# Kernel tuning notes

Measured on AMD Instinct MI355X. Metric: run time of the kernel, lower is better.

The kernel has to match this reference:

```python
import jax, jax.numpy as jnp
import numpy as np
from jax import lax

B, N, T_IN, F_IN = 64, 800, 15, 8
T_OUT = 12
H = 64
NC = 9
KS = [2, 2, 2, 3, 3, 3, 4, 4, 4]
DS = [1, 2, 4, 1, 2, 4, 1, 2, 4]


def setup_inputs() -> dict:
    key = jax.random.key(0)
    ks = jax.random.split(key, 16)
    s = 0.1
    f32 = jnp.float32
    inp = {}
    inp['A'] = jnp.zeros((1,), f32)  # deprecated graph arg, unused
    inp['X'] = jax.random.normal(ks[0], (B, N, T_IN, F_IN), f32)
    # dilated conv weights grouped by kernel size (comps 0-2 k=2, 3-5 k=3, 6-8 k=4)
    inp['convw2'] = jax.random.normal(ks[1], (3, F_IN, F_IN, 2), f32) * s
    inp['convw3'] = jax.random.normal(ks[2], (3, F_IN, F_IN, 3), f32) * s
    inp['convw4'] = jax.random.normal(ks[3], (3, F_IN, F_IN, 4), f32) * s
    inp['convb'] = jax.random.normal(ks[4], (NC, F_IN), f32) * s
    # encoder GRU params (PyTorch layout: W_ih (3H,F), W_hh (3H,H))
    inp['enc_wih'] = jax.random.normal(ks[5], (NC, 3 * H, F_IN), f32) * s
    inp['enc_whh'] = jax.random.normal(ks[6], (NC, 3 * H, H), f32) * s
    inp['enc_bih'] = jax.random.normal(ks[7], (NC, 3 * H), f32) * s
    inp['enc_bhh'] = jax.random.normal(ks[8], (NC, 3 * H), f32) * s
    # decoder GRUCell params (input size 1)
    inp['dec_wih'] = jax.random.normal(ks[9], (NC, 3 * H, 1), f32) * s
    inp['dec_whh'] = jax.random.normal(ks[10], (NC, 3 * H, H), f32) * s
    inp['dec_bih'] = jax.random.normal(ks[11], (NC, 3 * H), f32) * s
    inp['dec_bhh'] = jax.random.normal(ks[12], (NC, 3 * H), f32) * s
    # per-comp readout Linear(H, 1)
    inp['lin_w'] = jax.random.normal(ks[13], (NC, 1, H), f32) * s
    inp['lin_b'] = jax.random.normal(ks[14], (NC, 1), f32) * s
    # node-wise component mixing embedding
    inp['embed'] = jax.random.normal(ks[15], (N, NC), f32)
    return inp


def gru_cell(x, h, wih, whh, bih, bhh):
    # PyTorch GRU semantics
    gi = x @ wih.T + bih  # (B, 3H)
    gh = h @ whh.T + bhh  # (B, 3H)
    ir, iz, in_ = jnp.split(gi, 3, axis=-1)
    hr, hz, hn = jnp.split(gh, 3, axis=-1)
    r = jax.nn.sigmoid(ir + hr)
    z = jax.nn.sigmoid(iz + hz)
    n = jnp.tanh(in_ + r * hn)
    return (1.0 - z) * n + z * h


def reference(A, X, convw2, convw3, convw4, convb, enc_wih, enc_whh, enc_bih,
              enc_bhh, dec_wih, dec_whh, dec_bih, dec_bhh, lin_w, lin_b, embed):
    del A  # deprecated in pure TS model
    Xf = X.reshape(-1, T_IN, F_IN)            # (B*N, T, F)
    xt = jnp.transpose(Xf, (0, 2, 1))         # (B*N, F, T) for conv NCH
    last0 = Xf[:, -1, 0:1]                    # X1[-1, :, 0] -> (B*N, 1)
    BN = Xf.shape[0]
    conv_ws = [convw2[0], convw2[1], convw2[2], convw3[0], convw3[1],
               convw3[2], convw4[0], convw4[1], convw4[2]]
    outs = []
    for r in range(NC):
        # dilated conv over time, VALID padding (length shrinks by d*(k-1))
        h = lax.conv_general_dilated(xt, conv_ws[r], (1,), 'VALID',
                                     rhs_dilation=(DS[r],),
                                     dimension_numbers=('NCH', 'OIH', 'NCH'))
        h = h + convb[r][None, :, None]
        seq = jnp.transpose(h, (2, 0, 1))     # time-major (L, B*N, F)

        ewih, ewhh, ebih, ebhh = enc_wih[r], enc_whh[r], enc_bih[r], enc_bhh[r]

        def enc_step(hc, x_t):
            return gru_cell(x_t, hc, ewih, ewhh, ebih, ebhh), None

        h_enc, _ = lax.scan(enc_step, jnp.zeros((BN, H), X.dtype), seq)

        dwih, dwhh, dbih, dbhh = dec_wih[r], dec_whh[r], dec_bih[r], dec_bhh[r]
        lw, lb = lin_w[r], lin_b[r]

        def dec_step(carry, _):
            hd, lv = carry
            hd = gru_cell(lv, hd, dwih, dwhh, dbih, dbhh)
            v = hd @ lw.T + lb                # (B*N, 1)
            # torch code feeds value.detach() back in
            return (hd, lax.stop_gradient(v)), v[:, 0]

        _, vals = lax.scan(dec_step, (h_enc, last0), None, length=T_OUT)
        outs.append(jnp.transpose(vals).reshape(B, N, T_OUT))  # (B, N, T_out)
    out = jnp.stack(outs, axis=-1)            # (B, N, T_out, NC)
    w = jax.nn.softmax(embed, axis=-1)        # (N, NC)
    return jnp.einsum('bntc,nc->bnt', out, w)
```

## Files before the change

kernel.cpp:

```cpp
#include <hip/hip_runtime.h>
#include <hip/hip_bf16.h>
#include <stdint.h>

typedef unsigned short u16;
typedef unsigned int   u32;
typedef float f32x4  __attribute__((ext_vector_type(4)));
typedef short bf16x8 __attribute__((ext_vector_type(8)));

#define NSEQ 800
#define TOUT 12
#define NC   9
#define LOG2E  1.44269504088896340736f
#define LOG2E2 2.88539008177792681472f

#define WIMG_STRIDE 73728
#define LDS_BHE 0
#define LDS_BXE 24576
#define LDS_BHD 36864
#define LDS_H   61440
#define LDS_TOTAL 77824
#define BIASE_OFF 663552
#define BIASD_OFF 672768
#define WGT_OFF   681984

__device__ __forceinline__ u16 f2bf(float f){ union{float f;u32 i;}v; v.f=f; u32 x=v.i; return (u16)((x + 0x7fffu + ((x>>16)&1u))>>16); }
__device__ __forceinline__ u32 pkbf(float a, float b){
  union{ __hip_bfloat162 h2; u32 u; } v;
  v.h2 = __float22bfloat162_rn(float2{a,b});
  return v.u;
}

union BXU { uint4 u; bf16x8 v; };

__global__ void prep_kernel(
  const float* __restrict__ cw2, const float* __restrict__ cw3, const float* __restrict__ cw4,
  const float* __restrict__ cbv,
  const float* __restrict__ Ewih, const float* __restrict__ Ewhh,
  const float* __restrict__ Ebih, const float* __restrict__ Ebhh,
  const float* __restrict__ Dwih, const float* __restrict__ Dwhh,
  const float* __restrict__ Dbih, const float* __restrict__ Dbhh,
  const float* __restrict__ emb,
  char* __restrict__ ws)
{
  const int r = blockIdx.x;
  const int tid = threadIdx.x;
  const int K = (r<3) ? 2 : ((r<6) ? 3 : 4);
  char* wimg = ws + (size_t)r*WIMG_STRIDE;

  const float* ewhh = Ewhh + (size_t)r*192*64;
  const float* dwhh = Dwhh + (size_t)r*192*64;
  #pragma unroll 1
  for (int s = tid; s < 1536; s += 512){
    int g = s >> 6, fl = s & 63;
    int ks = g/12, nt = g%12;
    int col = nt*16 + (fl&15);
    float sc = (nt<8) ? LOG2E : LOG2E2;
    u32 we[4] = {0,0,0,0}, wd[4] = {0,0,0,0};
    #pragma unroll
    for (int j=0;j<8;j++){
      int hid = ((j&3)<<4) | (ks*8 + (fl>>4)*2 + (j>>2));
      we[j>>1] |= (u32)f2bf(sc * ewhh[col*64 + hid]) << ((j&1)*16);
      wd[j>>1] |= (u32)f2bf(sc * dwhh[col*64 + hid]) << ((j&1)*16);
    }
    *(uint4*)(wimg + LDS_BHE + s*16) = uint4{we[0],we[1],we[2],we[3]};
    *(uint4*)(wimg + LDS_BHD + s*16) = uint4{wd[0],wd[1],wd[2],wd[3]};
  }
  const float* wih = Ewih + r*192*8;
  const float* cw  = (r<3) ? (cw2 + r*128) : (r<6) ? (cw3 + (r-3)*192) : (cw4 + (r-6)*256);
  #pragma unroll 1
  for (int s = tid; s < 768; s += 512){
    int g = s >> 6, fl = s & 63;
    int col = g*16 + (fl&15);
    int tap = fl>>4;
    float sc = (g<8) ? LOG2E : LOG2E2;
    u32 w[4] = {0,0,0,0};
    if (tap < K){
      #pragma unroll
      for (int j=0;j<8;j++){
        float a = 0.f;
        #pragma unroll
        for (int o=0;o<8;o++) a += wih[col*8+o]*cw[(o*8+j)*K + tap];
        w[j>>1] |= (u32)f2bf(sc*a) << ((j&1)*16);
      }
    }
    *(uint4*)(wimg + LDS_BXE + s*16) = uint4{w[0],w[1],w[2],w[3]};
  }
  if (tid < 16){
    int n = tid;
    const float* bi = Ebih + r*192; const float* bh2 = Ebhh + r*192;
    const float* cb = cbv + r*8;
    float* be = (float*)(ws + BIASE_OFF) + ((size_t)r*16 + n)*16;
    #pragma unroll
    for (int ht=0; ht<4; ht++){
      int hid = ht*16 + n;
      float cR=0.f,cZ=0.f,cN=0.f;
      #pragma unroll
      for (int o=0;o<8;o++){
        cR += wih[hid*8+o]*cb[o];
        cZ += wih[(64+hid)*8+o]*cb[o];
        cN += wih[(128+hid)*8+o]*cb[o];
      }
      be[ht]    = LOG2E  * (bi[hid]     + bh2[hid]     + cR);
      be[4+ht]  = LOG2E  * (bi[64+hid]  + bh2[64+hid]  + cZ);
      be[8+ht]  = LOG2E2 * (bi[128+hid]                + cN);
      be[12+ht] = LOG2E2 *                bh2[128+hid];
    }
  } else if (tid < 32){
    int n = tid - 16;
    const float* bi = Dbih + r*192; const float* bh2 = Dbhh + r*192;
    float* bd = (float*)(ws + BIASD_OFF) + ((size_t)r*16 + n)*16;
    #pragma unroll
    for (int ht=0; ht<4; ht++){
      int hid = ht*16 + n;
      bd[ht]    = LOG2E  * (bi[hid]     + bh2[hid]);
      bd[4+ht]  = LOG2E  * (bi[64+hid]  + bh2[64+hid]);
      bd[8+ht]  = LOG2E2 *  bi[128+hid];
      bd[12+ht] = LOG2E2 *  bh2[128+hid];
    }
  }
  if (r == 0){
    float* wg = (float*)(ws + WGT_OFF);
    #pragma unroll 1
    for (int nb = tid; nb < NSEQ; nb += 512){
      float e[NC], mx = -1e30f;
      #pragma unroll
      for (int c=0;c<NC;c++){ e[c] = emb[nb*NC+c]; mx = fmaxf(mx, e[c]); }
      float sm = 0.f;
      #pragma unroll
      for (int c=0;c<NC;c++){ e[c] = __expf(e[c]-mx); sm += e[c]; }
      float inv = 1.f/sm;
      #pragma unroll
      for (int c=0;c<NC;c++) wg[nb*NC+c] = e[c]*inv;
    }
  }
}

__global__ __launch_bounds__(512, 2) void rnn_kernel(
  const float* __restrict__ X,
  const float* __restrict__ Dwih,
  const float* __restrict__ Lw, const float* __restrict__ Lb,
  const char* __restrict__ ws,
  float* __restrict__ out)
{
  __shared__ char LDSC[LDS_TOTAL];
  const int tid = threadIdx.x;
  const int wv  = tid >> 6;
  const int l   = tid & 63;
  const int q   = l >> 4;
  const int n   = l & 15;
  const int r   = blockIdx.y;
  const int seqb = blockIdx.x*128 + wv*16;

  const int Kc[NC]={2,2,2,3,3,3,4,4,4};
  const int Dc[NC]={1,2,4,1,2,4,1,2,4};
  const int K = Kc[r], D = Dc[r];
  const int L = 15 - (K-1)*D;

  const int HB = LDS_H + wv*2048;
  *(uint4*)(LDSC + HB + l*32)      = uint4{0,0,0,0};
  *(uint4*)(LDSC + HB + l*32 + 16) = uint4{0,0,0,0};

  {
    const uint4* src = (const uint4*)(ws + (size_t)r*WIMG_STRIDE);
    #pragma unroll 1
    for (int it=0; it<8; it++){
      int idx = it*512 + tid;
      if (idx < 3840) *(uint4*)(LDSC + idx*16) = src[idx];
    }
  }

  float bR4[4], bZ4[4], bNi4[4], bNh4[4];
  {
    const float* be = (const float*)(ws + BIASE_OFF) + ((size_t)r*16 + n)*16;
    float4 v0 = *(const float4*)(be);
    float4 v1 = *(const float4*)(be+4);
    float4 v2 = *(const float4*)(be+8);
    float4 v3 = *(const float4*)(be+12);
    bR4[0]=v0.x; bR4[1]=v0.y; bR4[2]=v0.z; bR4[3]=v0.w;
    bZ4[0]=v1.x; bZ4[1]=v1.y; bZ4[2]=v1.z; bZ4[3]=v1.w;
    bNi4[0]=v2.x; bNi4[1]=v2.y; bNi4[2]=v2.z; bNi4[3]=v2.w;
    bNh4[0]=v3.x; bNh4[1]=v3.y; bNh4[2]=v3.z; bNh4[3]=v3.w;
  }

  float hO[4][4];
  #pragma unroll
  for (int ht=0;ht<4;ht++) for (int i=0;i<4;i++) hO[ht][i]=0.f;

  const int ra0 = HB + n*128 + (((  q + n)&7)<<4);
  const int ra1 = HB + n*128 + (((4+q + n)&7)<<4);
  int wa[4];
  #pragma unroll
  for (int i=0;i<4;i++){
    int seq = q*4+i;
    wa[i] = HB + seq*128 + ((((n>>1) + seq)&7)<<4) + ((n&1)<<3);
  }

#define POINTWISE(aR_,aZ_,aNi_,aNh_,HT) \
    _Pragma("unroll") \
    for (int i=0;i<4;i++){ \
      float Er = __builtin_amdgcn_exp2f(-aR_[i]); \
      float rr = __builtin_amdgcn_rcpf(1.f + Er); \
      float y  = aNi_[i] + rr*aNh_[i]; \
      float En = __builtin_amdgcn_exp2f(y); \
      float Ez = __builtin_amdgcn_exp2f(-aZ_[i]); \
      float h  = hO[HT][i]; \
      float e1 = En + 1.f; \
      float den = e1 + e1*Ez; \
      float num = En*(Ez+h) + (h-Ez); \
      float hn = num * __builtin_amdgcn_rcpf(den); \
      hO[HT][i] = hn; \
      if (HT==0)      hsv[i] = hn; \
      else if (HT==1) pk01[i] = pkbf(hsv[i], hn); \
      else if (HT==2) hsv[i] = hn; \
      else            pk23[i] = pkbf(hsv[i], hn); \
    }

  auto step_core = [&](bf16x8 ax){
    bf16x8 a0 = *(const bf16x8*)(LDSC + ra0);
    bf16x8 a1 = *(const bf16x8*)(LDSC + ra1);
    float hsv[4]; u32 pk01[4], pk23[4];
    #pragma unroll
    for (int ht=0; ht<4; ht++){
      bf16x8 bR0 = *(const bf16x8*)(LDSC + LDS_BHE + ((      ht)*64 + l)*16);
      bf16x8 bR1 = *(const bf16x8*)(LDSC + LDS_BHE + ((12  + ht)*64 + l)*16);
      bf16x8 bZ0 = *(const bf16x8*)(LDSC + LDS_BHE + (( 4 + ht)*64 + l)*16);
      bf16x8 bZ1 = *(const bf16x8*)(LDSC + LDS_BHE + ((16  + ht)*64 + l)*16);
      bf16x8 bN0 = *(const bf16x8*)(LDSC + LDS_BHE + (( 8 + ht)*64 + l)*16);
      bf16x8 bN1 = *(const bf16x8*)(LDSC + LDS_BHE + ((20  + ht)*64 + l)*16);
      bf16x8 xR  = *(const bf16x8*)(LDSC + LDS_BXE + ((      ht)*64 + l)*16);
      bf16x8 xZ  = *(const bf16x8*)(LDSC + LDS_BXE + (( 4 + ht)*64 + l)*16);
      bf16x8 xN  = *(const bf16x8*)(LDSC + LDS_BXE + (( 8 + ht)*64 + l)*16);
      f32x4 aR  = f32x4{bR4[ht],bR4[ht],bR4[ht],bR4[ht]};
      f32x4 aZ  = f32x4{bZ4[ht],bZ4[ht],bZ4[ht],bZ4[ht]};
      f32x4 aNi = f32x4{bNi4[ht],bNi4[ht],bNi4[ht],bNi4[ht]};
      f32x4 aNh = f32x4{bNh4[ht],bNh4[ht],bNh4[ht],bNh4[ht]};
      aR = __builtin_amdgcn_mfma_f32_16x16x32_bf16(a0, bR0, aR,0,0,0);
      aR = __builtin_amdgcn_mfma_f32_16x16x32_bf16(a1, bR1, aR,0,0,0);
      aR = __builtin_amdgcn_mfma_f32_16x16x32_bf16(ax, xR,  aR,0,0,0);
      aZ = __builtin_amdgcn_mfma_f32_16x16x32_bf16(a0, bZ0, aZ,0,0,0);
      aZ = __builtin_amdgcn_mfma_f32_16x16x32_bf16(a1, bZ1, aZ,0,0,0);
      aZ = __builtin_amdgcn_mfma_f32_16x16x32_bf16(ax, xZ,  aZ,0,0,0);
      aNh= __builtin_amdgcn_mfma_f32_16x16x32_bf16(a0, bN0, aNh,0,0,0);
      aNh= __builtin_amdgcn_mfma_f32_16x16x32_bf16(a1, bN1, aNh,0,0,0);
      aNi= __builtin_amdgcn_mfma_f32_16x16x32_bf16(ax, xN,  aNi,0,0,0);
      POINTWISE(aR,aZ,aNi,aNh,ht)
    }
    #pragma unroll
    for (int i=0;i<4;i++){
      uint2 wv2; wv2.x = pk01[i]; wv2.y = pk23[i];
      *(uint2*)(LDSC + wa[i]) = wv2;
    }
  };

  const float* xb = X + (size_t)(seqb + n)*120 + ((q<K)? q:0)*D*8;
  __syncthreads();
  #pragma unroll 1
  for (int t=0; t<L; t++){
    float4 v0 = *(const float4*)(xb + t*8);
    float4 v1 = *(const float4*)(xb + t*8 + 4);
    BXU a;
    a.u.x = __builtin_amdgcn_perm(__float_as_uint(v0.y), __float_as_uint(v0.x), 0x07060302u);
    a.u.y = __builtin_amdgcn_perm(__float_as_uint(v0.w), __float_as_uint(v0.z), 0x07060302u);
    a.u.z = __builtin_amdgcn_perm(__float_as_uint(v1.y), __float_as_uint(v1.x), 0x07060302u);
    a.u.w = __builtin_amdgcn_perm(__float_as_uint(v1.w), __float_as_uint(v1.z), 0x07060302u);
    step_core(a.v);
  }

  {
    const float* bd = (const float*)(ws + BIASD_OFF) + ((size_t)r*16 + n)*16;
    float4 v0 = *(const float4*)(bd);
    float4 v1 = *(const float4*)(bd+4);
    float4 v2 = *(const float4*)(bd+8);
    float4 v3 = *(const float4*)(bd+12);
    bR4[0]=v0.x; bR4[1]=v0.y; bR4[2]=v0.z; bR4[3]=v0.w;
    bZ4[0]=v1.x; bZ4[1]=v1.y; bZ4[2]=v1.z; bZ4[3]=v1.w;
    bNi4[0]=v2.x; bNi4[1]=v2.y; bNi4[2]=v2.z; bNi4[3]=v2.w;
    bNh4[0]=v3.x; bNh4[1]=v3.y; bNh4[2]=v3.z; bNh4[3]=v3.w;
  }
  float dwR[4], dwZ[4], dwN[4];
  {
    const float* dwih = Dwih + r*192;
    #pragma unroll
    for (int ht=0; ht<4; ht++){
      int hid = ht*16 + n;
      dwR[ht] = LOG2E  * dwih[hid];
      dwZ[ht] = LOG2E  * dwih[64+hid];
      dwN[ht] = LOG2E2 * dwih[128+hid];
    }
  }
  float lwr[4];
  #pragma unroll
  for (int ht=0; ht<4; ht++) lwr[ht] = Lw[r*64 + ht*16 + n];
  const float lb_ = Lb[r];
  const float wgt = ((const float*)(ws + WGT_OFF))[((seqb + q*4 + (n&3)) % NSEQ)*NC + r];
  f32x4 lvv;
  #pragma unroll
  for (int i=0;i<4;i++) lvv[i] = X[(size_t)(seqb + q*4 + i)*120 + 112];

  #pragma unroll 1
  for (int t=0; t<TOUT; t++){
    {
      bf16x8 a0 = *(const bf16x8*)(LDSC + ra0);
      bf16x8 a1 = *(const bf16x8*)(LDSC + ra1);
      float hsv[4]; u32 pk01[4], pk23[4];
      #pragma unroll
      for (int ht=0; ht<4; ht++){
        bf16x8 bR0 = *(const bf16x8*)(LDSC + LDS_BHD + ((      ht)*64 + l)*16);
        bf16x8 bR1 = *(const bf16x8*)(LDSC + LDS_BHD + ((12  + ht)*64 + l)*16);
        bf16x8 bZ0 = *(const bf16x8*)(LDSC + LDS_BHD + (( 4 + ht)*64 + l)*16);
        bf16x8 bZ1 = *(const bf16x8*)(LDSC + LDS_BHD + ((16  + ht)*64 + l)*16);
        bf16x8 bN0 = *(const bf16x8*)(LDSC + LDS_BHD + (( 8 + ht)*64 + l)*16);
        bf16x8 bN1 = *(const bf16x8*)(LDSC + LDS_BHD + ((20  + ht)*64 + l)*16);
        f32x4 aR, aZ, aNi, aNh;
        #pragma unroll
        for (int i=0;i<4;i++){
          aR[i]  = bR4[ht]  + lvv[i]*dwR[ht];
          aZ[i]  = bZ4[ht]  + lvv[i]*dwZ[ht];
          aNi[i] = bNi4[ht] + lvv[i]*dwN[ht];
          aNh[i] = bNh4[ht];
        }
        aR = __builtin_amdgcn_mfma_f32_16x16x32_bf16(a0, bR0, aR,0,0,0);
        aR = __builtin_amdgcn_mfma_f32_16x16x32_bf16(a1, bR1, aR,0,0,0);
        aZ = __builtin_amdgcn_mfma_f32_16x16x32_bf16(a0, bZ0, aZ,0,0,0);
        aZ = __builtin_amdgcn_mfma_f32_16x16x32_bf16(a1, bZ1, aZ,0,0,0);
        aNh= __builtin_amdgcn_mfma_f32_16x16x32_bf16(a0, bN0, aNh,0,0,0);
        aNh= __builtin_amdgcn_mfma_f32_16x16x32_bf16(a1, bN1, aNh,0,0,0);
        POINTWISE(aR,aZ,aNi,aNh,ht)
      }
      #pragma unroll
      for (int i=0;i<4;i++){
        uint2 wv2; wv2.x = pk01[i]; wv2.y = pk23[i];
        *(uint2*)(LDSC + wa[i]) = wv2;
      }
    }
    float p[4];
    #pragma unroll
    for (int i=0;i<4;i++)
      p[i] = hO[0][i]*lwr[0] + hO[1][i]*lwr[1] + hO[2][i]*lwr[2] + hO[3][i]*lwr[3];
    #pragma unroll
    for (int m=1; m<16; m<<=1){
      #pragma unroll
      for (int i=0;i<4;i++) p[i] += __shfl_xor(p[i], m, 64);
    }
    #pragma unroll
    for (int i=0;i<4;i++) lvv[i] = p[i] + lb_;
    if (n < 4){
      float vout = (n&2) ? ((n&1)? lvv[3] : lvv[2]) : ((n&1)? lvv[1] : lvv[0]);
      atomicAdd(out + (size_t)(seqb + q*4 + n)*TOUT + t, wgt*vout);
    }
  }
}

extern "C" void kernel_launch(void* const* d_in, const int* in_sizes, int n_in,
                              void* d_out, int out_size, void* d_ws, size_t ws_size,
                              hipStream_t stream)
{
  float* out = (float*)d_out;
  hipMemsetAsync(out, 0, (size_t)out_size*sizeof(float), stream);

  prep_kernel<<<dim3(NC), 512, 0, stream>>>(
    (const float*)d_in[2], (const float*)d_in[3], (const float*)d_in[4],
    (const float*)d_in[5],
    (const float*)d_in[6], (const float*)d_in[7], (const float*)d_in[8], (const float*)d_in[9],
    (const float*)d_in[10],(const float*)d_in[11],(const float*)d_in[12],(const float*)d_in[13],
    (const float*)d_in[16],
    (char*)d_ws);

  dim3 g(NSEQ*64/128, NC);
  rnn_kernel<<<g, 512, 0, stream>>>(
    (const float*)d_in[1],
    (const float*)d_in[10],
    (const float*)d_in[14], (const float*)d_in[15],
    (const char*)d_ws,
    out);
}
```

Baseline: 755.7 us.

## Halve block size and reuse one LDS region for encoder and decoder weights

The encoder and decoder recurrent weight images now share one LDS region. The decoder weights are reloaded from workspace after the encoder loop, with barriers around the reload. This cuts LDS per block from about 76KB to 44KB. Blocks shrink from 512 to 256 threads with launch bounds of 4 blocks per CU, doubling the grid, to raise occupancy and latency hiding. The costs are an extra global-to-LDS copy and two block barriers per block, plus twice as many encoder-weight loads overall.

```diff
diff --git a/kernel.cpp b/kernel.cpp
--- a/kernel.cpp
+++ b/kernel.cpp
@@ -14,11 +14,11 @@
 #define LOG2E2 2.88539008177792681472f
 
 #define WIMG_STRIDE 73728
-#define LDS_BHE 0
+#define WIMG_BHD 36864
+#define LDS_BH  0
 #define LDS_BXE 24576
-#define LDS_BHD 36864
-#define LDS_H   61440
-#define LDS_TOTAL 77824
+#define LDS_H   36864
+#define LDS_TOTAL 45056
 #define BIASE_OFF 663552
 #define BIASD_OFF 672768
 #define WGT_OFF   681984
@@ -62,8 +62,8 @@
       we[j>>1] |= (u32)f2bf(sc * ewhh[col*64 + hid]) << ((j&1)*16);
       wd[j>>1] |= (u32)f2bf(sc * dwhh[col*64 + hid]) << ((j&1)*16);
     }
-    *(uint4*)(wimg + LDS_BHE + s*16) = uint4{we[0],we[1],we[2],we[3]};
-    *(uint4*)(wimg + LDS_BHD + s*16) = uint4{wd[0],wd[1],wd[2],wd[3]};
+    *(uint4*)(wimg + LDS_BH + s*16)   = uint4{we[0],we[1],we[2],we[3]};
+    *(uint4*)(wimg + WIMG_BHD + s*16) = uint4{wd[0],wd[1],wd[2],wd[3]};
   }
   const float* wih = Ewih + r*192*8;
   const float* cw  = (r<3) ? (cw2 + r*128) : (r<6) ? (cw3 + (r-3)*192) : (cw4 + (r-6)*256);
@@ -135,7 +135,7 @@
   }
 }
 
-__global__ __launch_bounds__(512, 2) void rnn_kernel(
+__global__ __launch_bounds__(256, 4) void rnn_kernel(
   const float* __restrict__ X,
   const float* __restrict__ Dwih,
   const float* __restrict__ Lw, const float* __restrict__ Lb,
@@ -149,7 +149,7 @@
   const int q   = l >> 4;
   const int n   = l & 15;
   const int r   = blockIdx.y;
-  const int seqb = blockIdx.x*128 + wv*16;
+  const int seqb = blockIdx.x*64 + wv*16;
 
   const int Kc[NC]={2,2,2,3,3,3,4,4,4};
   const int Dc[NC]={1,2,4,1,2,4,1,2,4};
@@ -163,9 +163,9 @@
   {
     const uint4* src = (const uint4*)(ws + (size_t)r*WIMG_STRIDE);
     #pragma unroll 1
-    for (int it=0; it<8; it++){
-      int idx = it*512 + tid;
-      if (idx < 3840) *(uint4*)(LDSC + idx*16) = src[idx];
+    for (int it=0; it<9; it++){
+      int idx = it*256 + tid;
+      *(uint4*)(LDSC + idx*16) = src[idx];
     }
   }
 
@@ -221,12 +221,12 @@
     float hsv[4]; u32 pk01[4], pk23[4];
     #pragma unroll
     for (int ht=0; ht<4; ht++){
-      bf16x8 bR0 = *(const bf16x8*)(LDSC + LDS_BHE + ((      ht)*64 + l)*16);
-      bf16x8 bR1 = *(const bf16x8*)(LDSC + LDS_BHE + ((12  + ht)*64 + l)*16);
-      bf16x8 bZ0 = *(const bf16x8*)(LDSC + LDS_BHE + (( 4 + ht)*64 + l)*16);
-      bf16x8 bZ1 = *(const bf16x8*)(LDSC + LDS_BHE + ((16  + ht)*64 + l)*16);
-      bf16x8 bN0 = *(const bf16x8*)(LDSC + LDS_BHE + (( 8 + ht)*64 + l)*16);
-      bf16x8 bN1 = *(const bf16x8*)(LDSC + LDS_BHE + ((20  + ht)*64 + l)*16);
+      bf16x8 bR0 = *(const bf16x8*)(LDSC + LDS_BH + ((      ht)*64 + l)*16);
+      bf16x8 bR1 = *(const bf16x8*)(LDSC + LDS_BH + ((12  + ht)*64 + l)*16);
+      bf16x8 bZ0 = *(const bf16x8*)(LDSC + LDS_BH + (( 4 + ht)*64 + l)*16);
+      bf16x8 bZ1 = *(const bf16x8*)(LDSC + LDS_BH + ((16  + ht)*64 + l)*16);
+      bf16x8 bN0 = *(const bf16x8*)(LDSC + LDS_BH + (( 8 + ht)*64 + l)*16);
+      bf16x8 bN1 = *(const bf16x8*)(LDSC + LDS_BH + ((20  + ht)*64 + l)*16);
       bf16x8 xR  = *(const bf16x8*)(LDSC + LDS_BXE + ((      ht)*64 + l)*16);
       bf16x8 xZ  = *(const bf16x8*)(LDSC + LDS_BXE + (( 4 + ht)*64 + l)*16);
       bf16x8 xN  = *(const bf16x8*)(LDSC + LDS_BXE + (( 8 + ht)*64 + l)*16);
@@ -266,6 +266,15 @@
     step_core(a.v);
   }
 
+  __syncthreads();
+  {
+    const uint4* src = (const uint4*)(ws + (size_t)r*WIMG_STRIDE + WIMG_BHD);
+    #pragma unroll 1
+    for (int it=0; it<6; it++){
+      int idx = it*256 + tid;
+      *(uint4*)(LDSC + LDS_BH + idx*16) = src[idx];
+    }
+  }
   {
     const float* bd = (const float*)(ws + BIASD_OFF) + ((size_t)r*16 + n)*16;
     float4 v0 = *(const float4*)(bd);
@@ -296,6 +305,7 @@
   f32x4 lvv;
   #pragma unroll
   for (int i=0;i<4;i++) lvv[i] = X[(size_t)(seqb + q*4 + i)*120 + 112];
+  __syncthreads();
 
   #pragma unroll 1
   for (int t=0; t<TOUT; t++){
@@ -305,12 +315,12 @@
       float hsv[4]; u32 pk01[4], pk23[4];
       #pragma unroll
       for (int ht=0; ht<4; ht++){
-        bf16x8 bR0 = *(const bf16x8*)(LDSC + LDS_BHD + ((      ht)*64 + l)*16);
-        bf16x8 bR1 = *(const bf16x8*)(LDSC + LDS_BHD + ((12  + ht)*64 + l)*16);
-        bf16x8 bZ0 = *(const bf16x8*)(LDSC + LDS_BHD + (( 4 + ht)*64 + l)*16);
-        bf16x8 bZ1 = *(const bf16x8*)(LDSC + LDS_BHD + ((16  + ht)*64 + l)*16);
-        bf16x8 bN0 = *(const bf16x8*)(LDSC + LDS_BHD + (( 8 + ht)*64 + l)*16);
-        bf16x8 bN1 = *(const bf16x8*)(LDSC + LDS_BHD + ((20  + ht)*64 + l)*16);
+        bf16x8 bR0 = *(const bf16x8*)(LDSC + LDS_BH + ((      ht)*64 + l)*16);
+        bf16x8 bR1 = *(const bf16x8*)(LDSC + LDS_BH + ((12  + ht)*64 + l)*16);
+        bf16x8 bZ0 = *(const bf16x8*)(LDSC + LDS_BH + (( 4 + ht)*64 + l)*16);
+        bf16x8 bZ1 = *(const bf16x8*)(LDSC + LDS_BH + ((16  + ht)*64 + l)*16);
+        bf16x8 bN0 = *(const bf16x8*)(LDSC + LDS_BH + (( 8 + ht)*64 + l)*16);
+        bf16x8 bN1 = *(const bf16x8*)(LDSC + LDS_BH + ((20  + ht)*64 + l)*16);
         f32x4 aR, aZ, aNi, aNh;
         #pragma unroll
         for (int i=0;i<4;i++){
@@ -366,8 +376,8 @@
     (const float*)d_in[16],
     (char*)d_ws);
 
-  dim3 g(NSEQ*64/128, NC);
-  rnn_kernel<<<g, 512, 0, stream>>>(
+  dim3 g(NSEQ*64/64, NC);
+  rnn_kernel<<<g, 256, 0, stream>>>(
     (const float*)d_in[1],
     (const float*)d_in[10],
     (const float*)d_in[14], (const float*)d_in[15],
```

Measured after the change: 1.033 ms. 1.37x slower.
